# Kernel optimization log

Hardware: AMD Instinct MI355X
Metric: run time of the kernel (lower is better)

Reference implementation:

```python
import jax, jax.numpy as jnp
import numpy as np

B, S, H, A, F = 16, 512, 768, 12, 3072
DH = H // A  # 64
EPS = 1e-5

def layernorm(x, w, b):
    mu = jnp.mean(x, axis=-1, keepdims=True)
    var = jnp.mean(jnp.square(x - mu), axis=-1, keepdims=True)
    return (x - mu) * jax.lax.rsqrt(var + EPS) * w + b

def setup_inputs() -> dict:
    key = jax.random.key(0)
    ks = jax.random.split(key, 12)
    std = 0.02
    inp = {
        "X": jax.random.normal(ks[0], (B, S, H), jnp.float32),
        "mask": jax.random.randint(ks[1], (B, S), 0, 2, jnp.int32),
        "WQ": jax.random.normal(ks[2], (H, H), jnp.float32) * std,
        "bQ": jnp.zeros((H,), jnp.float32),
        "WK": jax.random.normal(ks[3], (H, H), jnp.float32) * std,
        "bK": jnp.zeros((H,), jnp.float32),
        "WV": jax.random.normal(ks[4], (H, H), jnp.float32) * std,
        "bV": jnp.zeros((H,), jnp.float32),
        "WO": jax.random.normal(ks[5], (H, H), jnp.float32) * std,
        "bO": jnp.zeros((H,), jnp.float32),
        "ln1_w": jnp.ones((H,), jnp.float32),
        "ln1_b": jnp.zeros((H,), jnp.float32),
        "W1": jax.random.normal(ks[6], (H, F), jnp.float32) * std,
        "b1": jnp.zeros((F,), jnp.float32),
        "W2": jax.random.normal(ks[7], (F, H), jnp.float32) * std,
        "b2": jnp.zeros((H,), jnp.float32),
        "ln2_w": jnp.ones((H,), jnp.float32),
        "ln2_b": jnp.zeros((H,), jnp.float32),
    }
    return inp

def reference(X, mask, WQ, bQ, WK, bK, WV, bV, WO, bO, ln1_w, ln1_b, W1, b1, W2, b2, ln2_w, ln2_b):
    # --- multi-head self-attention (pretrained-weights branch, faithful reshapes) ---
    Q = (X @ WQ + bQ).reshape(B, A, S, DH)
    K = (X @ WK + bK).reshape(B, A, S, DH)
    V = (X @ WV + bV).reshape(B, A, S, DH)
    scores = jnp.einsum('bhqd,bhkd->bhqk', Q, K) / jnp.sqrt(jnp.float32(DH))
    scores = jnp.where(mask[:, None, None, :] == 0, -jnp.inf, scores)
    attn = jax.nn.softmax(scores, axis=-1)
    Z = jnp.einsum('bhqk,bhkd->bhqd', attn, V).reshape(B, S, H)
    attn_out = Z @ WO + bO
    # residual + LN (dropout is identity in eval)
    X = layernorm(attn_out + X, ln1_w, ln1_b)
    # --- FFN with exact GELU ---
    ffn = jax.nn.gelu(X @ W1 + b1, approximate=False) @ W2 + b2
    X = layernorm(ffn + X, ln2_w, ln2_b)
    return X
```

## Files before the change

### kernel.cpp

```cpp
#include <hip/hip_runtime.h>
#include <hip/hip_bf16.h>


using bf16_t = __hip_bfloat16;
typedef __bf16 bf16x8 __attribute__((ext_vector_type(8)));
typedef float f32x4 __attribute__((ext_vector_type(4)));
typedef float f32x16 __attribute__((ext_vector_type(16)));

__device__ __forceinline__ float b2f(bf16_t v) { return __bfloat162float(v); }
__device__ __forceinline__ bf16_t f2b(float v) { return __float2bfloat16(v); }
__device__ __forceinline__ ushort f2bu(float v) { bf16_t b = f2b(v); return *(ushort*)&b; }

__device__ __forceinline__ void glds16(const ushort* g, ushort* l) {
    __builtin_amdgcn_global_load_lds(
        (const __attribute__((address_space(1))) unsigned int*)g,
        (__attribute__((address_space(3))) unsigned int*)l, 16, 0, 0);
}

__device__ __forceinline__ float gelu_f(float x) {
    float x2 = x * x;
    float y2 = 1.5957691216057308f * x * fmaf(0.044715f, x2, 1.0f);
    float e = __expf(y2);
    float t = 1.f - 2.f / (e + 1.f);
    return 0.5f * x * (1.f + t);
}

__device__ __forceinline__ void tr_tile(const float* __restrict__ in,
                                        bf16_t* __restrict__ out,
                                        int R, int C, int tx, int ty,
                                        float (*t)[65], int tid)
{
    int r0 = ty * 64, c0 = tx * 64;
    int tr = tid >> 6, tc = tid & 63;
#pragma unroll 4
    for (int i = 0; i < 16; ++i) {
        int r = i * 4 + tr;
        t[r][tc] = in[(size_t)(r0 + r) * C + c0 + tc];
    }
    __syncthreads();
#pragma unroll 4
    for (int i = 0; i < 16; ++i) {
        int r = i * 4 + tr;
        out[(size_t)(c0 + r) * R + r0 + tc] = f2b(t[tc][r]);
    }
}

__global__ __launch_bounds__(256) void prep_kernel(
    const float* __restrict__ WQ, const float* __restrict__ WK,
    const float* __restrict__ WV, const float* __restrict__ WO,
    const float* __restrict__ W1, const float* __restrict__ W2,
    const float* __restrict__ bQ, const float* __restrict__ bK,
    const float* __restrict__ bV, const float* __restrict__ X,
    bf16_t* __restrict__ Wqkv, bf16_t* __restrict__ WOt,
    bf16_t* __restrict__ W1t, bf16_t* __restrict__ W2t,
    float* __restrict__ bcat, bf16_t* __restrict__ Xb)
{
    __shared__ float t[64][65];
    const int blk = blockIdx.x, tid = threadIdx.x;
    if (blk < 576) {
        int m = blk / 144, tt = blk % 144;
        const float* in = (m == 0) ? WQ : (m == 1) ? WK : (m == 2) ? WV : WO;
        bf16_t* out = (m == 0) ? Wqkv : (m == 1) ? Wqkv + 589824
                    : (m == 2) ? Wqkv + 1179648 : WOt;
        tr_tile(in, out, 768, 768, tt % 12, tt / 12, t, tid);
    } else if (blk < 1152) {
        int tt = blk - 576;
        tr_tile(W1, W1t, 768, 3072, tt % 48, tt / 48, t, tid);
    } else if (blk < 1728) {
        int tt = blk - 1152;
        tr_tile(W2, W2t, 3072, 768, tt % 12, tt / 12, t, tid);
    } else if (blk == 1728) {
        for (int i = tid; i < 2304; i += 256)
            bcat[i] = (i < 768) ? bQ[i] : (i < 1536) ? bK[i - 768] : bV[i - 1536];
    } else {
        size_t i = ((size_t)(blk - 1729) * 256 + tid) * 8;
        float4 a = *(const float4*)(X + i);
        float4 b = *(const float4*)(X + i + 4);
#pragma unroll
        for (int j = 0; j < 4; ++j) {
            Xb[i + j]     = f2b(((const float*)&a)[j]);
            Xb[i + 4 + j] = f2b(((const float*)&b)[j]);
        }
    }
}

template <int EPI>
__global__ __launch_bounds__(512, 1) void gemm_2ph(
    const bf16_t* __restrict__ A, const bf16_t* __restrict__ Bt,
    const float* __restrict__ bias, const void* __restrict__ res,
    void* __restrict__ Cv, int K, int lda, int ldb, int ldc)
{
    extern __shared__ ushort lds[];
    const int tid = threadIdx.x;
    const int l31 = tid & 31, khalf = (tid >> 5) & 1;
    const int w = tid >> 6;
    const int wr = w >> 2, wc = w & 3;
    const int m0 = blockIdx.x * 256, n0 = blockIdx.y * 256;

    const int srow = tid >> 3;
    const int sg = (((tid & 7) ^ (srow & 7)) << 3);
    const ushort* gA = (const ushort*)A + (size_t)(m0 + srow) * lda + sg;
    const ushort* gB = (const ushort*)Bt + (size_t)(n0 + srow) * ldb + sg;
    const int dOff = tid * 8;

    f32x16 acc[4][2] = {};
    const int arow = wr * 128, brow = wc * 64;
    const int nk = K >> 6;

    STAGE_DEF:;
    auto STAGE = [&](int t, int cur) {
        ushort* buf = lds + cur * 32768;
        const size_t ko = (size_t)t << 6;
#pragma unroll
        for (int p = 0; p < 4; ++p)
            glds16(gA + ko + (size_t)(p * 64) * lda, buf + p * 4096 + dOff);
#pragma unroll
        for (int p = 0; p < 4; ++p)
            glds16(gB + ko + (size_t)(p * 64) * ldb, buf + 16384 + p * 4096 + dOff);
    };

    auto COMPUTE = [&](int cur) {
        const ushort* buf = lds + cur * 32768;
#pragma unroll
        for (int kk = 0; kk < 4; ++kk) {
            const int pc = (((kk * 2 + khalf) ^ (l31 & 7)) << 3);
            bf16x8 afr[4], bfr[2];
#pragma unroll
            for (int mi = 0; mi < 4; ++mi)
                afr[mi] = *(const bf16x8*)&buf[(arow + mi * 32 + l31) * 64 + pc];
#pragma unroll
            for (int ni = 0; ni < 2; ++ni)
                bfr[ni] = *(const bf16x8*)&buf[16384 + (brow + ni * 32 + l31) * 64 + pc];
#pragma unroll
            for (int mi = 0; mi < 4; ++mi)
#pragma unroll
                for (int ni = 0; ni < 2; ++ni)
                    acc[mi][ni] = __builtin_amdgcn_mfma_f32_32x32x16_bf16(bfr[ni], afr[mi], acc[mi][ni], 0, 0, 0);
        }
    };

    STAGE(0, 0);
    asm volatile("s_waitcnt vmcnt(0)" ::: "memory");
    __builtin_amdgcn_s_barrier();

    int cur = 0;
    for (int t = 0; t < nk - 1; ++t) {
        STAGE(t + 1, cur ^ 1);
        __builtin_amdgcn_s_setprio(1);
        COMPUTE(cur);
        __builtin_amdgcn_s_setprio(0);
        asm volatile("s_waitcnt vmcnt(0)" ::: "memory");
        __builtin_amdgcn_s_barrier();
        cur ^= 1;
    }
    COMPUTE(cur);

#pragma unroll
    for (int mi = 0; mi < 4; ++mi) {
        int m = m0 + arow + mi * 32 + l31;
#pragma unroll
        for (int ni = 0; ni < 2; ++ni) {
#pragma unroll
            for (int g = 0; g < 4; ++g) {
                int nb = n0 + brow + ni * 32 + 8 * g + 4 * khalf;
                float4 bv4 = *(const float4*)&bias[nb];
                float v[4];
#pragma unroll
                for (int r = 0; r < 4; ++r) v[r] = acc[mi][ni][g * 4 + r] + ((const float*)&bv4)[r];
                if constexpr (EPI == 1) {
#pragma unroll
                    for (int r = 0; r < 4; ++r) v[r] = gelu_f(v[r]);
                }
                ushort4 st;
                st.x = f2bu(v[0]); st.y = f2bu(v[1]); st.z = f2bu(v[2]); st.w = f2bu(v[3]);
                *(ushort4*)&((ushort*)Cv)[(size_t)m * ldc + nb] = st;
            }
        }
    }
}

template <int EPI, int NTILE>
__global__ __launch_bounds__(256) void gemm128(
    const bf16_t* __restrict__ A, const bf16_t* __restrict__ Bt,
    const float* __restrict__ bias, const void* __restrict__ res,
    void* __restrict__ Cv, int K, int lda, int ldb, int ldc)
{
    __shared__ ushort lA[128 * 64];
    __shared__ ushort lB[NTILE * 64];
    constexpr int NI = NTILE / 64;
    const int tid = threadIdx.x;
    const int l = tid & 63, w = tid >> 6;
    const int l31 = l & 31, khalf = l >> 5;
    const int m0 = blockIdx.x * 128, n0 = blockIdx.y * NTILE;

    const int srow = tid >> 3;
    const int sg = (((tid & 7) ^ (srow & 7)) << 3);
    const ushort* gA = (const ushort*)A + (size_t)(m0 + srow) * lda + sg;
    const ushort* gB = (const ushort*)Bt + (size_t)(n0 + srow) * ldb + sg;
    ushort* dA = lA + tid * 8;
    ushort* dB = lB + tid * 8;

    f32x16 acc[2][NI] = {};
    const int arow = (w & 1) * 64;
    const int brow = (w >> 1) * (NTILE / 2);

    for (int k0 = 0; k0 < K; k0 += 64) {
        __syncthreads();
        glds16(gA + k0,                      dA);
        glds16(gA + k0 + (size_t)32 * lda,   dA + 2048);
        glds16(gA + k0 + (size_t)64 * lda,   dA + 4096);
        glds16(gA + k0 + (size_t)96 * lda,   dA + 6144);
        glds16(gB + k0,                      dB);
        glds16(gB + k0 + (size_t)32 * ldb,   dB + 2048);
        if constexpr (NTILE == 128) {
            glds16(gB + k0 + (size_t)64 * ldb, dB + 4096);
            glds16(gB + k0 + (size_t)96 * ldb, dB + 6144);
        }
        __syncthreads();
#pragma unroll
        for (int kk = 0; kk < 4; ++kk) {
            const int pc = (((kk * 2 + khalf) ^ (l31 & 7)) << 3);
            bf16x8 bfr[NI];
#pragma unroll
            for (int ni = 0; ni < NI; ++ni)
                bfr[ni] = *(const bf16x8*)&lB[(brow + ni * 32 + l31) * 64 + pc];
#pragma unroll
            for (int mi = 0; mi < 2; ++mi) {
                bf16x8 afr = *(const bf16x8*)&lA[(arow + mi * 32 + l31) * 64 + pc];
#pragma unroll
                for (int ni = 0; ni < NI; ++ni)
                    acc[mi][ni] = __builtin_amdgcn_mfma_f32_32x32x16_bf16(bfr[ni], afr, acc[mi][ni], 0, 0, 0);
            }
        }
    }

#pragma unroll
    for (int mi = 0; mi < 2; ++mi) {
        int m = m0 + arow + mi * 32 + l31;
#pragma unroll
        for (int ni = 0; ni < NI; ++ni) {
#pragma unroll
            for (int g = 0; g < 4; ++g) {
                int nb = n0 + brow + ni * 32 + 8 * g + 4 * khalf;
                float4 bv4 = *(const float4*)&bias[nb];
                float v[4];
#pragma unroll
                for (int r = 0; r < 4; ++r) v[r] = acc[mi][ni][g * 4 + r] + ((const float*)&bv4)[r];
                if constexpr (EPI == 1) {
#pragma unroll
                    for (int r = 0; r < 4; ++r) v[r] = gelu_f(v[r]);
                } else if constexpr (EPI == 2) {
                    float4 r4 = *(const float4*)&((const float*)res)[(size_t)m * ldc + nb];
#pragma unroll
                    for (int r = 0; r < 4; ++r) v[r] += ((const float*)&r4)[r];
                } else if constexpr (EPI == 5) {
                    ushort4 rb = *(const ushort4*)&((const ushort*)res)[(size_t)m * ldc + nb];
#pragma unroll
                    for (int r = 0; r < 4; ++r) v[r] += b2f(*(const bf16_t*)&((const ushort*)&rb)[r]);
                }
                if constexpr (EPI == 5) {
                    *(float4*)&((float*)Cv)[(size_t)m * ldc + nb] = make_float4(v[0], v[1], v[2], v[3]);
                } else {
                    ushort4 st;
                    st.x = f2bu(v[0]); st.y = f2bu(v[1]); st.z = f2bu(v[2]); st.w = f2bu(v[3]);
                    if constexpr (EPI == 6) {
                        int seg = n0 / 768;
                        int nloc = (n0 % 768) + brow + ni * 32 + 8 * g + 4 * khalf;
                        if (seg < 2) {
                            bf16_t* Cseg = (bf16_t*)Cv + (size_t)seg * 6291456;
                            *(ushort4*)&((ushort*)Cseg)[(size_t)m * 768 + nloc] = st;
                        } else {
                            ushort* vt = (ushort*)res;
                            int fb = (m & 511) * 768 + nloc;
                            int h = (m >> 9) * 12 + (fb >> 15);
                            int d = fb & 63;
                            int s = (fb >> 6) & 511;
                            ushort* vh = vt + (size_t)h * 32768 + s;
                            vh[(size_t)(d + 0) * 512] = st.x;
                            vh[(size_t)(d + 1) * 512] = st.y;
                            vh[(size_t)(d + 2) * 512] = st.z;
                            vh[(size_t)(d + 3) * 512] = st.w;
                        }
                    } else {
                        *(ushort4*)&((ushort*)Cv)[(size_t)m * ldc + nb] = st;
                    }
                }
            }
        }
    }
}

__global__ __launch_bounds__(256) void flash_kernel(
    const bf16_t* __restrict__ Q, const bf16_t* __restrict__ Kx,
    const bf16_t* __restrict__ Vt, const int* __restrict__ mask,
    bf16_t* __restrict__ Z)
{
    __shared__ ushort lK[64 * 64];
    __shared__ ushort lV[64 * 64];
    __shared__ ushort lP[128 * 72];

    const int h = blockIdx.y;
    const int q0 = blockIdx.x * 128;
    const ushort* Qh = (const ushort*)Q + (size_t)h * 32768;
    const ushort* Kh = (const ushort*)Kx + (size_t)h * 32768;
    const ushort* Vh = (const ushort*)Vt + (size_t)h * 32768;
    const int* mk = mask + (h / 12) * 512;
    ushort* Zh = (ushort*)Z + (size_t)h * 32768;

    const int tid = threadIdx.x;
    const int l = tid & 63, w = tid >> 6;
    const int l16 = l & 15, quad = l >> 4;

    bf16x8 qfr[2][2];
#pragma unroll
    for (int mi = 0; mi < 2; ++mi)
#pragma unroll
        for (int kk = 0; kk < 2; ++kk)
            qfr[mi][kk] = *(const bf16x8*)(Qh + (size_t)(q0 + w * 32 + mi * 16 + l16) * 64 + kk * 32 + quad * 8);

    const int c8p = tid & 7;
    const int kr0 = tid >> 3;
    float m_i[2] = {-1e30f, -1e30f}, l_i[2] = {0.f, 0.f};
    f32x4 o4[2][4] = {};

    for (int kt = 0; kt < 8; ++kt) {
#pragma unroll
        for (int p = 0; p < 2; ++p) {
            int row = kr0 + p * 32;
            int c8l = c8p ^ (row & 7);
            glds16(Kh + (size_t)(kt * 64 + row) * 64 + c8l * 8, lK + (p * 256 + tid) * 8);
            glds16(Vh + (size_t)row * 512 + kt * 64 + c8l * 8, lV + (p * 256 + tid) * 8);
        }
        __syncthreads();

        f32x4 s4[2][4] = {};
#pragma unroll
        for (int kk = 0; kk < 2; ++kk) {
#pragma unroll
            for (int nt = 0; nt < 4; ++nt) {
                bf16x8 kfr = *(const bf16x8*)&lK[(nt * 16 + l16) * 64 + (((kk * 4 + quad) ^ (l16 & 7)) << 3)];
#pragma unroll
                for (int mi = 0; mi < 2; ++mi)
                    s4[mi][nt] = __builtin_amdgcn_mfma_f32_16x16x32_bf16(kfr, qfr[mi][kk], s4[mi][nt], 0, 0, 0);
            }
        }

        int4 m4[4];
#pragma unroll
        for (int nt = 0; nt < 4; ++nt) m4[nt] = *(const int4*)&mk[kt * 64 + nt * 16 + quad * 4];

#pragma unroll
        for (int mi = 0; mi < 2; ++mi) {
            float pv[4][4];
            float rm = -1e30f;
#pragma unroll
            for (int nt = 0; nt < 4; ++nt)
#pragma unroll
                for (int r = 0; r < 4; ++r) {
                    float v = (((const int*)&m4[nt])[r] == 0) ? -1e30f : s4[mi][nt][r] * 0.125f;
                    pv[nt][r] = v;
                    rm = fmaxf(rm, v);
                }
            rm = fmaxf(rm, __shfl_xor(rm, 16));
            rm = fmaxf(rm, __shfl_xor(rm, 32));
            float mn = fmaxf(m_i[mi], rm);
            float al = __expf(m_i[mi] - mn);
            float rs = 0.f;
#pragma unroll
            for (int nt = 0; nt < 4; ++nt)
#pragma unroll
                for (int r = 0; r < 4; ++r) {
                    float e = __expf(pv[nt][r] - mn);
                    pv[nt][r] = e;
                    rs += e;
                }
            rs += __shfl_xor(rs, 16);
            rs += __shfl_xor(rs, 32);
            l_i[mi] = l_i[mi] * al + rs;
            m_i[mi] = mn;
#pragma unroll
            for (int dt = 0; dt < 4; ++dt)
#pragma unroll
                for (int r = 0; r < 4; ++r) o4[mi][dt][r] *= al;

#pragma unroll
            for (int nt = 0; nt < 4; ++nt) {
                ushort4 st;
                st.x = f2bu(pv[nt][0]); st.y = f2bu(pv[nt][1]);
                st.z = f2bu(pv[nt][2]); st.w = f2bu(pv[nt][3]);
                *(ushort4*)&lP[(w * 32 + mi * 16 + l16) * 72 + nt * 16 + quad * 4] = st;
            }
        }
        __syncthreads();

#pragma unroll
        for (int kk = 0; kk < 2; ++kk) {
#pragma unroll
            for (int dt = 0; dt < 4; ++dt) {
                bf16x8 bvfr = *(const bf16x8*)&lV[(dt * 16 + l16) * 64 + (((kk * 4 + quad) ^ (l16 & 7)) << 3)];
#pragma unroll
                for (int mi = 0; mi < 2; ++mi) {
                    bf16x8 pafr = *(const bf16x8*)&lP[(w * 32 + mi * 16 + l16) * 72 + kk * 32 + quad * 8];
                    o4[mi][dt] = __builtin_amdgcn_mfma_f32_16x16x32_bf16(bvfr, pafr, o4[mi][dt], 0, 0, 0);
                }
            }
        }
        __syncthreads();
    }

#pragma unroll
    for (int mi = 0; mi < 2; ++mi) {
        float inv = 1.f / l_i[mi];
#pragma unroll
        for (int dt = 0; dt < 4; ++dt) {
            ushort4 st;
            st.x = f2bu(o4[mi][dt][0] * inv); st.y = f2bu(o4[mi][dt][1] * inv);
            st.z = f2bu(o4[mi][dt][2] * inv); st.w = f2bu(o4[mi][dt][3] * inv);
            *(ushort4*)&Zh[(size_t)(q0 + w * 32 + mi * 16 + l16) * 64 + dt * 16 + quad * 4] = st;
        }
    }
}

__device__ __forceinline__ float to_f(float v)  { return v; }
__device__ __forceinline__ float to_f(bf16_t v) { return b2f(v); }
__device__ __forceinline__ void from_f(float& d, float v)  { d = v; }
__device__ __forceinline__ void from_f(bf16_t& d, float v) { d = f2b(v); }

template <typename TI, typename TO>
__global__ __launch_bounds__(256) void layernorm_kernel(
    const TI* __restrict__ X, const float* __restrict__ w,
    const float* __restrict__ b, TO* __restrict__ out)
{
    const TI* x = X + (size_t)blockIdx.x * 768;
    TO* o = out + (size_t)blockIdx.x * 768;
    int t = threadIdx.x;
    float v[3];
    float s = 0.f, sq = 0.f;
#pragma unroll
    for (int i = 0; i < 3; ++i) {
        v[i] = to_f(x[t + i * 256]);
        s += v[i]; sq += v[i] * v[i];
    }
#pragma unroll
    for (int off = 32; off; off >>= 1) { s += __shfl_xor(s, off); sq += __shfl_xor(sq, off); }
    __shared__ float s1[4], s2[4];
    int wave = t >> 6, lane = t & 63;
    if (lane == 0) { s1[wave] = s; s2[wave] = sq; }
    __syncthreads();
    s  = s1[0] + s1[1] + s1[2] + s1[3];
    sq = s2[0] + s2[1] + s2[2] + s2[3];
    float mu  = s * (1.f / 768.f);
    float var = sq * (1.f / 768.f) - mu * mu;
    float rs  = rsqrtf(var + 1e-5f);
#pragma unroll
    for (int i = 0; i < 3; ++i)
        from_f(o[t + i * 256], (v[i] - mu) * rs * w[t + i * 256] + b[t + i * 256]);
}

extern "C" void kernel_launch(void* const* d_in, const int* in_sizes, int n_in,
                              void* d_out, int out_size, void* d_ws, size_t ws_size,
                              hipStream_t stream)
{
    const float* X    = (const float*)d_in[0];
    const int*   mask = (const int*)  d_in[1];
    const float* WQ   = (const float*)d_in[2];
    const float* bQ   = (const float*)d_in[3];
    const float* WK   = (const float*)d_in[4];
    const float* bK   = (const float*)d_in[5];
    const float* WV   = (const float*)d_in[6];
    const float* bV   = (const float*)d_in[7];
    const float* WO   = (const float*)d_in[8];
    const float* bO   = (const float*)d_in[9];
    const float* ln1w = (const float*)d_in[10];
    const float* ln1b = (const float*)d_in[11];
    const float* W1   = (const float*)d_in[12];
    const float* b1   = (const float*)d_in[13];
    const float* W2   = (const float*)d_in[14];
    const float* b2   = (const float*)d_in[15];
    const float* ln2w = (const float*)d_in[16];
    const float* ln2b = (const float*)d_in[17];
    float* out = (float*)d_out;

    bf16_t* ws   = (bf16_t*)d_ws;
    bf16_t* Wqkv = ws;
    bf16_t* WOt  = Wqkv + 1769472;
    bf16_t* W1t  = WOt + 589824;
    bf16_t* W2t  = W1t + 2359296;
    float*  bcat = (float*)(W2t + 2359296);
    bf16_t* Qb   = W2t + 2359296 + 4608;
    bf16_t* Kb   = Qb + 6291456;
    bf16_t* Vb   = Kb + 6291456;
    bf16_t* Xb   = Vb + 6291456;
    bf16_t* Vt   = Xb + 6291456;
    bf16_t* Zb = Qb;
    bf16_t* Y1 = Xb;
    bf16_t* X1 = Qb;
    bf16_t* Hb = Kb;

    (void)hipFuncSetAttribute(reinterpret_cast<const void*>(&gemm_2ph<1>),
                              hipFuncAttributeMaxDynamicSharedMemorySize, 131072);

    prep_kernel<<<4801, 256, 0, stream>>>(WQ, WK, WV, WO, W1, W2, bQ, bK, bV, X,
                                          Wqkv, WOt, W1t, W2t, bcat, Xb);

    gemm128<6, 128><<<dim3(64, 18), 256, 0, stream>>>(Xb, Wqkv, bcat, Vt, Qb,
                                                      768, 768, 768, 768);

    flash_kernel<<<dim3(4, 192), 256, 0, stream>>>(Qb, Kb, Vt, mask, Zb);

    gemm128<2, 64><<<dim3(64, 12), 256, 0, stream>>>(Zb, WOt, bO, X, Y1,
                                                     768, 768, 768, 768);
    layernorm_kernel<bf16_t, bf16_t><<<8192, 256, 0, stream>>>(Y1, ln1w, ln1b, X1);

    gemm_2ph<1><<<dim3(32, 12), 512, 131072, stream>>>(X1, W1t, b1, nullptr, Hb,
                                                       768, 768, 768, 3072);
    gemm128<5, 64><<<dim3(64, 12), 256, 0, stream>>>(Hb, W2t, b2, X1, out,
                                                     3072, 3072, 3072, 768);
    layernorm_kernel<float, float><<<8192, 256, 0, stream>>>(out, ln2w, ln2b, out);
}
```

Measured before the change: 371.8 us.

## Restructure 256x256 GEMM into 8-phase pipelined schedule and use it for QKV

Replaces the two-phase double-buffered 256x256 GEMM with an eight-phase schedule. Each K tile is split into half-tile A/B loads that are interleaved with quadrant MFMA blocks, using barriers, sched_barrier and setprio to overlap global-to-LDS copies with compute. The QKV projection moves from the 128x128 kernel to this 256x256 kernel, with the fused Q/K/V scatter epilogue moved along with it. The fine-grained phases add many barriers, and the QKV grid shrinks to 288 blocks, which may underfill the CUs.

```diff
diff --git a/kernel.cpp b/kernel.cpp
--- a/kernel.cpp
+++ b/kernel.cpp
@@ -85,7 +85,7 @@
 }
 
 template <int EPI>
-__global__ __launch_bounds__(512, 1) void gemm_2ph(
+__global__ __launch_bounds__(512, 1) void gemm_8ph(
     const bf16_t* __restrict__ A, const bf16_t* __restrict__ Bt,
     const float* __restrict__ bias, const void* __restrict__ res,
     void* __restrict__ Cv, int K, int lda, int ldb, int ldc)
@@ -97,72 +97,118 @@
     const int wr = w >> 2, wc = w & 3;
     const int m0 = blockIdx.x * 256, n0 = blockIdx.y * 256;
 
-    const int srow = tid >> 3;
-    const int sg = (((tid & 7) ^ (srow & 7)) << 3);
-    const ushort* gA = (const ushort*)A + (size_t)(m0 + srow) * lda + sg;
-    const ushort* gB = (const ushort*)Bt + (size_t)(n0 + srow) * ldb + sg;
+    const int s = tid >> 3;
+    const int c = (((tid & 7) ^ (s & 7)) << 3);
+    const ushort* pA[4];
+    pA[0] = (const ushort*)A + (size_t)(m0 + s)       * lda + c;
+    pA[1] = (const ushort*)A + (size_t)(m0 + 128 + s) * lda + c;
+    pA[2] = (const ushort*)A + (size_t)(m0 + 64 + s)  * lda + c;
+    pA[3] = (const ushort*)A + (size_t)(m0 + 192 + s) * lda + c;
+    const int nbs = ((s >> 5) << 6) + (s & 31);
+    const ushort* pB[4];
+    pB[0] = (const ushort*)Bt + (size_t)(n0 + nbs)        * ldb + c;
+    pB[1] = (const ushort*)Bt + (size_t)(n0 + 128 + nbs)  * ldb + c;
+    pB[2] = (const ushort*)Bt + (size_t)(n0 + nbs + 32)   * ldb + c;
+    pB[3] = (const ushort*)Bt + (size_t)(n0 + 128 + nbs + 32) * ldb + c;
     const int dOff = tid * 8;
 
     f32x16 acc[4][2] = {};
-    const int arow = wr * 128, brow = wc * 64;
     const int nk = K >> 6;
 
-    STAGE_DEF:;
-    auto STAGE = [&](int t, int cur) {
-        ushort* buf = lds + cur * 32768;
-        const size_t ko = (size_t)t << 6;
-#pragma unroll
-        for (int p = 0; p < 4; ++p)
-            glds16(gA + ko + (size_t)(p * 64) * lda, buf + p * 4096 + dOff);
-#pragma unroll
-        for (int p = 0; p < 4; ++p)
-            glds16(gB + ko + (size_t)(p * 64) * ldb, buf + 16384 + p * 4096 + dOff);
+    auto SA = [&](int bo, int u, int kt) {
+        ushort* d = lds + bo + u * 8192 + dOff;
+        glds16(pA[2 * u]     + (size_t)kt * 64, d);
+        glds16(pA[2 * u + 1] + (size_t)kt * 64, d + 4096);
     };
-
-    auto COMPUTE = [&](int cur) {
-        const ushort* buf = lds + cur * 32768;
+    auto SB = [&](int bo, int u, int kt) {
+        ushort* d = lds + bo + 16384 + u * 8192 + dOff;
+        glds16(pB[2 * u]     + (size_t)kt * 64, d);
+        glds16(pB[2 * u + 1] + (size_t)kt * 64, d + 4096);
+    };
+
+    bf16x8 a[8], b0[4], b1[4];
+    auto RDA = [&](int mh, int bo) {
+#pragma unroll
+        for (int m2 = 0; m2 < 2; ++m2)
+#pragma unroll
+            for (int kk = 0; kk < 4; ++kk) {
+                int ar = mh * 128 + wr * 64 + m2 * 32 + l31;
+                a[m2 * 4 + kk] = *(const bf16x8*)&lds[bo + ar * 64 + (((kk * 2 + khalf) ^ (l31 & 7)) << 3)];
+            }
+    };
+    auto RDB = [&](int ni, int bo, bf16x8* b) {
+        int br = ni * 128 + wc * 32 + l31;
+#pragma unroll
+        for (int kk = 0; kk < 4; ++kk)
+            b[kk] = *(const bf16x8*)&lds[bo + 16384 + br * 64 + (((kk * 2 + khalf) ^ (l31 & 7)) << 3)];
+    };
+    auto MM = [&](int mh, int ni, bf16x8* b) {
 #pragma unroll
         for (int kk = 0; kk < 4; ++kk) {
-            const int pc = (((kk * 2 + khalf) ^ (l31 & 7)) << 3);
-            bf16x8 afr[4], bfr[2];
-#pragma unroll
-            for (int mi = 0; mi < 4; ++mi)
-                afr[mi] = *(const bf16x8*)&buf[(arow + mi * 32 + l31) * 64 + pc];
-#pragma unroll
-            for (int ni = 0; ni < 2; ++ni)
-                bfr[ni] = *(const bf16x8*)&buf[16384 + (brow + ni * 32 + l31) * 64 + pc];
-#pragma unroll
-            for (int mi = 0; mi < 4; ++mi)
-#pragma unroll
-                for (int ni = 0; ni < 2; ++ni)
-                    acc[mi][ni] = __builtin_amdgcn_mfma_f32_32x32x16_bf16(bfr[ni], afr[mi], acc[mi][ni], 0, 0, 0);
+            acc[mh * 2 + 0][ni] = __builtin_amdgcn_mfma_f32_32x32x16_bf16(b[kk], a[kk],     acc[mh * 2 + 0][ni], 0, 0, 0);
+            acc[mh * 2 + 1][ni] = __builtin_amdgcn_mfma_f32_32x32x16_bf16(b[kk], a[4 + kk], acc[mh * 2 + 1][ni], 0, 0, 0);
         }
     };
 
-    STAGE(0, 0);
-    asm volatile("s_waitcnt vmcnt(0)" ::: "memory");
+#define PH_SYNC() do { __builtin_amdgcn_s_barrier(); \
+    asm volatile("s_waitcnt lgkmcnt(0)" ::: "memory"); \
+    __builtin_amdgcn_sched_barrier(0); \
+    __builtin_amdgcn_s_setprio(1); } while (0)
+#define PH_END() do { __builtin_amdgcn_s_setprio(0); \
+    __builtin_amdgcn_s_barrier(); } while (0)
+
+    SA(0, 0, 0); SB(0, 0, 0); SA(0, 1, 0); SB(0, 1, 0);
+    SA(32768, 0, 1); SB(32768, 0, 1);
+    asm volatile("s_waitcnt vmcnt(4)" ::: "memory");
     __builtin_amdgcn_s_barrier();
 
-    int cur = 0;
-    for (int t = 0; t < nk - 1; ++t) {
-        STAGE(t + 1, cur ^ 1);
-        __builtin_amdgcn_s_setprio(1);
-        COMPUTE(cur);
-        __builtin_amdgcn_s_setprio(0);
-        asm volatile("s_waitcnt vmcnt(0)" ::: "memory");
+    for (int T = 0; T < nk; T += 2) {
+        const bool n2 = (T + 2) < nk;
+        SA(32768, 1, T + 1);
+        RDA(0, 0); RDB(0, 0, b0);
+        PH_SYNC(); MM(0, 0, b0); PH_END();
+        SB(32768, 1, T + 1);
+        RDB(1, 0, b1);
+        PH_SYNC(); MM(0, 1, b1); PH_END();
+        if (n2) SA(0, 0, T + 2);
+        RDA(1, 0);
+        PH_SYNC(); MM(1, 0, b0); PH_END();
+        if (n2) SB(0, 0, T + 2);
         __builtin_amdgcn_s_barrier();
-        cur ^= 1;
-    }
-    COMPUTE(cur);
+        asm volatile("s_waitcnt lgkmcnt(0)" ::: "memory");
+        __builtin_amdgcn_sched_barrier(0);
+        __builtin_amdgcn_s_setprio(1); MM(1, 1, b1); __builtin_amdgcn_s_setprio(0);
+        if (n2) asm volatile("s_waitcnt vmcnt(4)" ::: "memory");
+        else    asm volatile("s_waitcnt vmcnt(0)" ::: "memory");
+        __builtin_amdgcn_s_barrier();
+        if (n2) SA(0, 1, T + 2);
+        RDA(0, 32768); RDB(0, 32768, b0);
+        PH_SYNC(); MM(0, 0, b0); PH_END();
+        if (n2) SB(0, 1, T + 2);
+        RDB(1, 32768, b1);
+        PH_SYNC(); MM(0, 1, b1); PH_END();
+        if (n2) SA(32768, 0, T + 3);
+        RDA(1, 32768);
+        PH_SYNC(); MM(1, 0, b0); PH_END();
+        if (n2) SB(32768, 0, T + 3);
+        __builtin_amdgcn_s_barrier();
+        asm volatile("s_waitcnt lgkmcnt(0)" ::: "memory");
+        __builtin_amdgcn_sched_barrier(0);
+        __builtin_amdgcn_s_setprio(1); MM(1, 1, b1); __builtin_amdgcn_s_setprio(0);
+        if (n2) asm volatile("s_waitcnt vmcnt(4)" ::: "memory");
+        __builtin_amdgcn_s_barrier();
+    }
+#undef PH_SYNC
+#undef PH_END
 
 #pragma unroll
     for (int mi = 0; mi < 4; ++mi) {
-        int m = m0 + arow + mi * 32 + l31;
+        int m = m0 + wr * 128 + mi * 32 + l31;
 #pragma unroll
         for (int ni = 0; ni < 2; ++ni) {
 #pragma unroll
             for (int g = 0; g < 4; ++g) {
-                int nb = n0 + brow + ni * 32 + 8 * g + 4 * khalf;
+                int nb = n0 + wc * 64 + ni * 32 + 8 * g + 4 * khalf;
                 float4 bv4 = *(const float4*)&bias[nb];
                 float v[4];
 #pragma unroll
@@ -173,7 +219,27 @@
                 }
                 ushort4 st;
                 st.x = f2bu(v[0]); st.y = f2bu(v[1]); st.z = f2bu(v[2]); st.w = f2bu(v[3]);
-                *(ushort4*)&((ushort*)Cv)[(size_t)m * ldc + nb] = st;
+                if constexpr (EPI == 6) {
+                    int seg = n0 / 768;
+                    int nloc = (n0 % 768) + wc * 64 + ni * 32 + 8 * g + 4 * khalf;
+                    if (seg < 2) {
+                        bf16_t* Cseg = (bf16_t*)Cv + (size_t)seg * 6291456;
+                        *(ushort4*)&((ushort*)Cseg)[(size_t)m * 768 + nloc] = st;
+                    } else {
+                        ushort* vt = (ushort*)res;
+                        int fb = (m & 511) * 768 + nloc;
+                        int h = (m >> 9) * 12 + (fb >> 15);
+                        int d = fb & 63;
+                        int sx = (fb >> 6) & 511;
+                        ushort* vh = vt + (size_t)h * 32768 + sx;
+                        vh[(size_t)(d + 0) * 512] = st.x;
+                        vh[(size_t)(d + 1) * 512] = st.y;
+                        vh[(size_t)(d + 2) * 512] = st.z;
+                        vh[(size_t)(d + 3) * 512] = st.w;
+                    }
+                } else {
+                    *(ushort4*)&((ushort*)Cv)[(size_t)m * ldc + nb] = st;
+                }
             }
         }
     }
@@ -263,27 +329,7 @@
                 } else {
                     ushort4 st;
                     st.x = f2bu(v[0]); st.y = f2bu(v[1]); st.z = f2bu(v[2]); st.w = f2bu(v[3]);
-                    if constexpr (EPI == 6) {
-                        int seg = n0 / 768;
-                        int nloc = (n0 % 768) + brow + ni * 32 + 8 * g + 4 * khalf;
-                        if (seg < 2) {
-                            bf16_t* Cseg = (bf16_t*)Cv + (size_t)seg * 6291456;
-                            *(ushort4*)&((ushort*)Cseg)[(size_t)m * 768 + nloc] = st;
-                        } else {
-                            ushort* vt = (ushort*)res;
-                            int fb = (m & 511) * 768 + nloc;
-                            int h = (m >> 9) * 12 + (fb >> 15);
-                            int d = fb & 63;
-                            int s = (fb >> 6) & 511;
-                            ushort* vh = vt + (size_t)h * 32768 + s;
-                            vh[(size_t)(d + 0) * 512] = st.x;
-                            vh[(size_t)(d + 1) * 512] = st.y;
-                            vh[(size_t)(d + 2) * 512] = st.z;
-                            vh[(size_t)(d + 3) * 512] = st.w;
-                        }
-                    } else {
-                        *(ushort4*)&((ushort*)Cv)[(size_t)m * ldc + nb] = st;
-                    }
+                    *(ushort4*)&((ushort*)Cv)[(size_t)m * ldc + nb] = st;
                 }
             }
         }
@@ -497,13 +543,15 @@
     bf16_t* X1 = Qb;
     bf16_t* Hb = Kb;
 
-    (void)hipFuncSetAttribute(reinterpret_cast<const void*>(&gemm_2ph<1>),
+    (void)hipFuncSetAttribute(reinterpret_cast<const void*>(&gemm_8ph<6>),
+                              hipFuncAttributeMaxDynamicSharedMemorySize, 131072);
+    (void)hipFuncSetAttribute(reinterpret_cast<const void*>(&gemm_8ph<1>),
                               hipFuncAttributeMaxDynamicSharedMemorySize, 131072);
 
     prep_kernel<<<4801, 256, 0, stream>>>(WQ, WK, WV, WO, W1, W2, bQ, bK, bV, X,
                                           Wqkv, WOt, W1t, W2t, bcat, Xb);
 
-    gemm128<6, 128><<<dim3(64, 18), 256, 0, stream>>>(Xb, Wqkv, bcat, Vt, Qb,
+    gemm_8ph<6><<<dim3(32, 9), 512, 131072, stream>>>(Xb, Wqkv, bcat, Vt, Qb,
                                                       768, 768, 768, 768);
 
     flash_kernel<<<dim3(4, 192), 256, 0, stream>>>(Qb, Kb, Vt, mask, Zb);
@@ -512,7 +560,7 @@
                                                      768, 768, 768, 768);
     layernorm_kernel<bf16_t, bf16_t><<<8192, 256, 0, stream>>>(Y1, ln1w, ln1b, X1);
 
-    gemm_2ph<1><<<dim3(32, 12), 512, 131072, stream>>>(X1, W1t, b1, nullptr, Hb,
+    gemm_8ph<1><<<dim3(32, 12), 512, 131072, stream>>>(X1, W1t, b1, nullptr, Hb,
                                                        768, 768, 768, 3072);
     gemm128<5, 64><<<dim3(64, 12), 256, 0, stream>>>(Hb, W2t, b2, X1, out,
                                                      3072, 3072, 3072, 768);
```

Measured after the change: 396.9 us. +6.8%, slower.
